# Kernel optimization log

Hardware: AMD Instinct MI355X
Metric: run time of the kernel (lower is better)

The kernel has to match this reference:

```python
import jax, jax.numpy as jnp
import numpy as np
from jax.scipy.special import logsumexp

# Module hyperparameters
N_PARTS = 128
BATCH = 1024
# Entropic-regularized solver settings (differentiable surrogate for the
# cvxpylayers LP solve; eps small relative to O(1) eta-phi distances)
EPS = 0.02
ITERS = 100
LOG_FLOOR = 1e-30  # avoid log(0) for zero-mass dummy particles


def setup_inputs() -> dict:
    key = jax.random.key(0)
    k1, k2 = jax.random.split(key)
    # [B, n_parts, 3]: features (eta, phi, pt); uniform fill keeps pt > 0
    jets1 = jax.random.uniform(k1, (BATCH, N_PARTS, 3), dtype=jnp.float32)
    jets2 = jax.random.uniform(k2, (BATCH, N_PARTS, 3), dtype=jnp.float32)
    return {"jets1": jets1, "jets2": jets2}


def _sinkhorn_flow(C, loga, logb):
    """Batched log-domain Sinkhorn. C: [B,N,M], loga: [B,N], logb: [B,M].
    Returns the transport plan (flow) [B,N,M] with marginals ~ (a, b)."""
    f = jnp.zeros_like(loga)
    g = jnp.zeros_like(logb)

    def step(carry, _):
        f, g = carry
        f = EPS * (loga - logsumexp((g[:, None, :] - C) / EPS, axis=2))
        g = EPS * (logb - logsumexp((f[:, :, None] - C) / EPS, axis=1))
        return (f, g), None

    (f, g), _ = jax.lax.scan(step, (f, g), None, length=ITERS)
    return jnp.exp((f[:, :, None] + g[:, None, :] - C) / EPS)


def reference(jets1, jets2):
    n = jets1.shape[1]
    # Pairwise eta-phi ground distances: [B, n, n]
    diffs = -(jets1[:, :, None, :2] - jets2[:, None, :, :2]) + 1e-12
    dists = jnp.linalg.norm(diffs, axis=3)
    # pt weights (LP marginals)
    w1 = jets1[:, :, 2]
    w2 = jets2[:, :, 2]
    E1 = jnp.sum(w1, axis=1)
    E2 = jnp.sum(w2, axis=1)
    EabsDiff = jnp.abs(E2 - E1)
    # Partial OT (total mass = min(E1,E2), row/col sums <= w) is made balanced
    # by adding one zero-cost dummy particle per side absorbing the excess mass.
    a = jnp.concatenate([w1, jnp.maximum(E2 - E1, 0.0)[:, None]], axis=1)  # [B, n+1]
    b = jnp.concatenate([w2, jnp.maximum(E1 - E2, 0.0)[:, None]], axis=1)  # [B, n+1]
    Cp = jnp.pad(dists, ((0, 0), (0, 1), (0, 1)))  # dummy row/col have zero cost
    loga = jnp.log(jnp.maximum(a, LOG_FLOOR))
    logb = jnp.log(jnp.maximum(b, LOG_FLOOR))
    flow = _sinkhorn_flow(Cp, loga, logb)  # [B, n+1, n+1]
    # EMD = transport cost over real particles + energy-difference penalty
    emds = jnp.sum(dists * flow[:, :n, :n], axis=(1, 2)) + EabsDiff  # [B]
    return emds
```

## Files before the change

kernel.cpp:

```cpp
#include <hip/hip_runtime.h>

#define NP    128
#define NITER 100
#define BLK   512
#define RSC   72.13475204444817f
#define IRSC  0.013862943611198906f

typedef __attribute__((ext_vector_type(8))) short bf16x8;
typedef __attribute__((ext_vector_type(4))) float f32x4;

template<int CTRL>
__device__ __forceinline__ float dppf(float x) {
  return __int_as_float(__builtin_amdgcn_update_dpp(
      0, __float_as_int(x), CTRL, 0xf, 0xf, false));
}
__device__ __forceinline__ float rowsum16(float x) {
  x += dppf<0x121>(x); x += dppf<0x122>(x);
  x += dppf<0x124>(x); x += dppf<0x128>(x);
  return x;
}
__device__ __forceinline__ float wsum64(float x) {
  #pragma unroll
  for (int s = 1; s < 64; s <<= 1) x += __shfl_xor(x, s);
  return x;
}
__device__ __forceinline__ unsigned short f2bf(float f) {
  unsigned u = __float_as_uint(f);
  u += 0x7fffu + ((u >> 16) & 1u);
  return (unsigned short)(u >> 16);
}
__device__ __forceinline__ float bf2f(unsigned short h) {
  return __uint_as_float(((unsigned)h) << 16);
}

__global__ __launch_bounds__(BLK, 4) void emd_sinkhorn(
    const float* __restrict__ j1g, const float* __restrict__ j2g,
    float* __restrict__ out)
{
  __shared__ __align__(16) float x1s[NP], y1s[NP], x2s[NP], y2s[NP];
  __shared__ __align__(16) float ah[NP + 4], bh[NP + 4];
  __shared__ __align__(16) unsigned short Qlds[NP], Plds[NP];
  __shared__ __align__(16) float sumQ[8], sumP[8];
  __shared__ float red[8];

  const int t  = threadIdx.x;
  const int l  = t & 63;
  const int wv = t >> 6;
  const int lg = l >> 4;
  const int li = l & 15;
  const int b  = blockIdx.x;
  const float* J1 = j1g + (size_t)b * (NP * 3);
  const float* J2 = j2g + (size_t)b * (NP * 3);

  if (t < NP) {
    x1s[t] = J1[3*t]; y1s[t] = J1[3*t+1]; ah[t] = J1[3*t+2];
    x2s[t] = J2[3*t]; y2s[t] = J2[3*t+1]; bh[t] = J2[3*t+2];
  }
  __syncthreads();

  const float e1 = wsum64(ah[l] + ah[l + 64]);
  const float e2 = wsum64(bh[l] + bh[l + 64]);
  const float dE = fabsf(e2 - e1);
  __syncthreads();

  if (t < NP) { ah[t] = fmaxf(ah[t], 1e-30f); bh[t] = fmaxf(bh[t], 1e-30f); }
  if (t == 0) {
    ah[NP] = fmaxf(fmaxf(e2 - e1, 0.0f), 1e-30f);
    bh[NP] = fmaxf(fmaxf(e1 - e2, 0.0f), 1e-30f);
  }
  if (t < NP) Qlds[t] = 0x3F80;
  if (l == 0) sumQ[wv] = 16.0f;
  __syncthreads();

  const float aslk = ah[NP], bslk = bh[NP];
  float a4[4];
  #pragma unroll
  for (int q = 0; q < 4; ++q) a4[q] = ah[16*wv + lg*4 + q];
  const float bcol = bh[16*wv + li];

  bf16x8 KA[4], KB[4];
  {
    const int nA = 16*wv + li;
    const int mB = 16*wv + li;
    const float x1A = x1s[nA], y1A = y1s[nA];
    const float x2B = x2s[mB], y2B = y2s[mB];
    #pragma unroll
    for (int c = 0; c < 4; ++c) {
      #pragma unroll
      for (int i = 0; i < 8; ++i) {
        const int k = 32*c + lg*8 + i;
        float dx = x2s[k] - x1A + 1e-12f;
        float dy = y2s[k] - y1A + 1e-12f;
        KA[c][i] = (short)f2bf(
            __builtin_amdgcn_exp2f(-__builtin_sqrtf(dx*dx + dy*dy) * RSC));
        dx = x2B - x1s[k] + 1e-12f;
        dy = y2B - y1s[k] + 1e-12f;
        KB[c][i] = (short)f2bf(
            __builtin_amdgcn_exp2f(-__builtin_sqrtf(dx*dx + dy*dy) * RSC));
      }
    }
  }

  float q128 = 1.0f, p128;
  bf16x8 qf[4];

  for (int it = 0; it < NITER; ++it) {
    #pragma unroll
    for (int c = 0; c < 4; ++c)
      qf[c] = *(const bf16x8*)&Qlds[c*32 + lg*8];
    const float4 s0 = *(const float4*)&sumQ[0];
    const float4 s1 = *(const float4*)&sumQ[4];
    const float SQ = ((s0.x + s0.y) + (s0.z + s0.w))
                   + ((s1.x + s1.y) + (s1.z + s1.w));
    f32x4 acc = {0.f, 0.f, 0.f, 0.f};
    #pragma unroll
    for (int c = 0; c < 4; ++c)
      acc = __builtin_amdgcn_mfma_f32_16x16x32_bf16(KA[c], qf[c], acc, 0, 0, 0);
    p128 = aslk * __builtin_amdgcn_rcpf(SQ + q128);
    float pv[4];
    #pragma unroll
    for (int q = 0; q < 4; ++q)
      pv[q] = a4[q] * __builtin_amdgcn_rcpf(acc[q] + q128);
    float ps = (pv[0] + pv[1]) + (pv[2] + pv[3]);
    ps += __shfl_xor(ps, 16);
    ps += __shfl_xor(ps, 32);
    if (l == 0) sumP[wv] = ps;
    if (li == 0) {
      uint2 pk;
      pk.x = (unsigned)f2bf(pv[0]) | ((unsigned)f2bf(pv[1]) << 16);
      pk.y = (unsigned)f2bf(pv[2]) | ((unsigned)f2bf(pv[3]) << 16);
      *(uint2*)&Plds[16*wv + lg*4] = pk;
    }
    __syncthreads();

    bf16x8 pf[4];
    #pragma unroll
    for (int c = 0; c < 4; ++c)
      pf[c] = *(const bf16x8*)&Plds[c*32 + lg*8];
    const float4 t0 = *(const float4*)&sumP[0];
    const float4 t1 = *(const float4*)&sumP[4];
    const float SP = ((t0.x + t0.y) + (t0.z + t0.w))
                   + ((t1.x + t1.y) + (t1.z + t1.w));
    f32x4 acc2 = {0.f, 0.f, 0.f, 0.f};
    #pragma unroll
    for (int c = 0; c < 4; ++c)
      acc2 = __builtin_amdgcn_mfma_f32_16x16x32_bf16(pf[c], KB[c], acc2, 0, 0, 0);
    q128 = bslk * __builtin_amdgcn_rcpf(SP + p128);
    const float qv = bcol * __builtin_amdgcn_rcpf(acc2[0] + p128);
    const float qs = rowsum16(qv);
    if (l == 0) sumQ[wv] = qs;
    if (l < 16) Qlds[16*wv + li] = f2bf(qv);
    __syncthreads();
  }

  const float Pn = bf2f(Plds[16*wv + li]);
  #pragma unroll
  for (int c = 0; c < 4; ++c)
    qf[c] = *(const bf16x8*)&Qlds[c*32 + lg*8];
  float acc = 0.0f;
  #pragma unroll
  for (int c = 0; c < 4; ++c) {
    #pragma unroll
    for (int i = 0; i < 8; ++i) {
      const float kk = bf2f((unsigned short)KA[c][i]);
      const float qm = bf2f((unsigned short)qf[c][i]);
      const float d  = -__builtin_amdgcn_logf(kk) * IRSC;
      acc = fmaf(d, (Pn * kk) * qm, acc);
    }
  }
  acc = wsum64(acc);
  if (l == 0) red[wv] = acc;
  __syncthreads();
  if (t == 0)
    out[b] = (((red[0] + red[1]) + (red[2] + red[3]))
            + ((red[4] + red[5]) + (red[6] + red[7]))) + dE;
}

extern "C" void kernel_launch(void* const* d_in, const int* in_sizes, int n_in,
                              void* d_out, int out_size, void* d_ws, size_t ws_size,
                              hipStream_t stream) {
  const float* j1 = (const float*)d_in[0];
  const float* j2 = (const float*)d_in[1];
  float* outp = (float*)d_out;
  const int batch = in_sizes[0] / (NP * 3);
  hipLaunchKernelGGL(emd_sinkhorn, dim3(batch), dim3(BLK), 0, stream,
                     j1, j2, outp);
}
```

Baseline: 192.7 us.

## Run each batch's Sinkhorn loop in a single wavefront holding full kernel matrices

Each batch element moves from an 8-wave block to a single 64-lane wave that keeps both full 128x128 bf16 Gibbs kernels in registers (KA and KB, 32 bf16x8 each). Each iteration issues 32 MFMAs per half-step in that one wave. Cross-wave shared-memory reductions are replaced by wave-local shuffles, and barriers become cheap single-wave syncs. The cost is much higher register pressure (about 256 VGPRs just for the kernels), possible spilling, and fewer waves per CU, so MFMA latency may be exposed with less parallelism available to hide it.

After: 236.7 us. 1.23x slower.

```diff
diff --git a/kernel.cpp b/kernel.cpp
--- a/kernel.cpp
+++ b/kernel.cpp
@@ -2,178 +2,177 @@
 
 #define NP    128
 #define NITER 100
-#define BLK   512
 #define RSC   72.13475204444817f
 #define IRSC  0.013862943611198906f
 
 typedef __attribute__((ext_vector_type(8))) short bf16x8;
 typedef __attribute__((ext_vector_type(4))) float f32x4;
 
-template<int CTRL>
-__device__ __forceinline__ float dppf(float x) {
-  return __int_as_float(__builtin_amdgcn_update_dpp(
-      0, __float_as_int(x), CTRL, 0xf, 0xf, false));
-}
-__device__ __forceinline__ float rowsum16(float x) {
-  x += dppf<0x121>(x); x += dppf<0x122>(x);
-  x += dppf<0x124>(x); x += dppf<0x128>(x);
-  return x;
-}
 __device__ __forceinline__ float wsum64(float x) {
   #pragma unroll
   for (int s = 1; s < 64; s <<= 1) x += __shfl_xor(x, s);
   return x;
+}
+__device__ __forceinline__ float bf2f(unsigned short h) {
+  return __uint_as_float(((unsigned)h) << 16);
 }
 __device__ __forceinline__ unsigned short f2bf(float f) {
   unsigned u = __float_as_uint(f);
   u += 0x7fffu + ((u >> 16) & 1u);
   return (unsigned short)(u >> 16);
 }
-__device__ __forceinline__ float bf2f(unsigned short h) {
-  return __uint_as_float(((unsigned)h) << 16);
-}
 
-__global__ __launch_bounds__(BLK, 4) void emd_sinkhorn(
+__global__ __launch_bounds__(64, 1) void emd_sinkhorn(
     const float* __restrict__ j1g, const float* __restrict__ j2g,
     float* __restrict__ out)
 {
   __shared__ __align__(16) float x1s[NP], y1s[NP], x2s[NP], y2s[NP];
-  __shared__ __align__(16) float ah[NP + 4], bh[NP + 4];
-  __shared__ __align__(16) unsigned short Qlds[NP], Plds[NP];
-  __shared__ __align__(16) float sumQ[8], sumP[8];
-  __shared__ float red[8];
+  __shared__ __align__(16) float ahs[NP], bhs[NP];
+  __shared__ __align__(16) float Slds[NP];
+  __shared__ __align__(16) unsigned short Plds[NP];
+  __shared__ __align__(16) unsigned short Qlds[NP];
 
-  const int t  = threadIdx.x;
-  const int l  = t & 63;
-  const int wv = t >> 6;
+  const int l  = threadIdx.x;
   const int lg = l >> 4;
   const int li = l & 15;
   const int b  = blockIdx.x;
   const float* J1 = j1g + (size_t)b * (NP * 3);
   const float* J2 = j2g + (size_t)b * (NP * 3);
 
-  if (t < NP) {
-    x1s[t] = J1[3*t]; y1s[t] = J1[3*t+1]; ah[t] = J1[3*t+2];
-    x2s[t] = J2[3*t]; y2s[t] = J2[3*t+1]; bh[t] = J2[3*t+2];
+  #pragma unroll
+  for (int k = l; k < NP; k += 64) {
+    x1s[k] = J1[3*k]; y1s[k] = J1[3*k+1]; ahs[k] = J1[3*k+2];
+    x2s[k] = J2[3*k]; y2s[k] = J2[3*k+1]; bhs[k] = J2[3*k+2];
   }
   __syncthreads();
 
-  const float e1 = wsum64(ah[l] + ah[l + 64]);
-  const float e2 = wsum64(bh[l] + bh[l + 64]);
+  const float e1 = wsum64(ahs[l] + ahs[l + 64]);
+  const float e2 = wsum64(bhs[l] + bhs[l + 64]);
   const float dE = fabsf(e2 - e1);
-  __syncthreads();
+  const float aslk = fmaxf(fmaxf(e2 - e1, 0.0f), 1e-30f);
+  const float bslk = fmaxf(fmaxf(e1 - e2, 0.0f), 1e-30f);
+  const float2 araw = *(const float2*)&ahs[2*l];
+  const float2 braw = *(const float2*)&bhs[2*l];
+  const float ah0 = fmaxf(araw.x, 1e-30f), ah1 = fmaxf(araw.y, 1e-30f);
+  const float bh0 = fmaxf(braw.x, 1e-30f), bh1 = fmaxf(braw.y, 1e-30f);
 
-  if (t < NP) { ah[t] = fmaxf(ah[t], 1e-30f); bh[t] = fmaxf(bh[t], 1e-30f); }
-  if (t == 0) {
-    ah[NP] = fmaxf(fmaxf(e2 - e1, 0.0f), 1e-30f);
-    bh[NP] = fmaxf(fmaxf(e1 - e2, 0.0f), 1e-30f);
+  bf16x8 KA[8][4], KB[8][4];
+  #pragma unroll
+  for (int rt = 0; rt < 8; ++rt) {
+    const float xr = x1s[16*rt + li], yr = y1s[16*rt + li];
+    #pragma unroll
+    for (int kt = 0; kt < 4; ++kt) {
+      #pragma unroll
+      for (int i2 = 0; i2 < 8; ++i2) {
+        const int k = 32*kt + 8*lg + i2;
+        const float dx = x2s[k] - xr + 1e-12f;
+        const float dy = y2s[k] - yr + 1e-12f;
+        KA[rt][kt][i2] = (short)f2bf(
+            __builtin_amdgcn_exp2f(-__builtin_sqrtf(dx*dx + dy*dy) * RSC));
+      }
+    }
   }
-  if (t < NP) Qlds[t] = 0x3F80;
-  if (l == 0) sumQ[wv] = 16.0f;
-  __syncthreads();
-
-  const float aslk = ah[NP], bslk = bh[NP];
-  float a4[4];
   #pragma unroll
-  for (int q = 0; q < 4; ++q) a4[q] = ah[16*wv + lg*4 + q];
-  const float bcol = bh[16*wv + li];
-
-  bf16x8 KA[4], KB[4];
-  {
-    const int nA = 16*wv + li;
-    const int mB = 16*wv + li;
-    const float x1A = x1s[nA], y1A = y1s[nA];
-    const float x2B = x2s[mB], y2B = y2s[mB];
+  for (int ct = 0; ct < 8; ++ct) {
+    const float xc = x2s[16*ct + li], yc = y2s[16*ct + li];
     #pragma unroll
-    for (int c = 0; c < 4; ++c) {
+    for (int kt = 0; kt < 4; ++kt) {
       #pragma unroll
-      for (int i = 0; i < 8; ++i) {
-        const int k = 32*c + lg*8 + i;
-        float dx = x2s[k] - x1A + 1e-12f;
-        float dy = y2s[k] - y1A + 1e-12f;
-        KA[c][i] = (short)f2bf(
-            __builtin_amdgcn_exp2f(-__builtin_sqrtf(dx*dx + dy*dy) * RSC));
-        dx = x2B - x1s[k] + 1e-12f;
-        dy = y2B - y1s[k] + 1e-12f;
-        KB[c][i] = (short)f2bf(
+      for (int i2 = 0; i2 < 8; ++i2) {
+        const int k = 32*kt + 8*lg + i2;
+        const float dx = xc - x1s[k] + 1e-12f;
+        const float dy = yc - y1s[k] + 1e-12f;
+        KB[ct][kt][i2] = (short)f2bf(
             __builtin_amdgcn_exp2f(-__builtin_sqrtf(dx*dx + dy*dy) * RSC));
       }
     }
   }
 
-  float q128 = 1.0f, p128;
-  bf16x8 qf[4];
+  ((unsigned*)Qlds)[l] = 0x3F803F80u;
+  float SQ = 128.0f, q128 = 1.0f;
+  __syncthreads();
 
   for (int it = 0; it < NITER; ++it) {
+    const float p128 = aslk * __builtin_amdgcn_rcpf(SQ + q128);
+
+    bf16x8 qf[4];
     #pragma unroll
-    for (int c = 0; c < 4; ++c)
-      qf[c] = *(const bf16x8*)&Qlds[c*32 + lg*8];
-    const float4 s0 = *(const float4*)&sumQ[0];
-    const float4 s1 = *(const float4*)&sumQ[4];
-    const float SQ = ((s0.x + s0.y) + (s0.z + s0.w))
-                   + ((s1.x + s1.y) + (s1.z + s1.w));
-    f32x4 acc = {0.f, 0.f, 0.f, 0.f};
+    for (int kt = 0; kt < 4; ++kt)
+      qf[kt] = *(const bf16x8*)((const char*)Qlds + 64*kt + 16*lg);
+    f32x4 acc[8];
     #pragma unroll
-    for (int c = 0; c < 4; ++c)
-      acc = __builtin_amdgcn_mfma_f32_16x16x32_bf16(KA[c], qf[c], acc, 0, 0, 0);
-    p128 = aslk * __builtin_amdgcn_rcpf(SQ + q128);
-    float pv[4];
-    #pragma unroll
-    for (int q = 0; q < 4; ++q)
-      pv[q] = a4[q] * __builtin_amdgcn_rcpf(acc[q] + q128);
-    float ps = (pv[0] + pv[1]) + (pv[2] + pv[3]);
-    ps += __shfl_xor(ps, 16);
-    ps += __shfl_xor(ps, 32);
-    if (l == 0) sumP[wv] = ps;
+    for (int rt = 0; rt < 8; ++rt) {
+      acc[rt] = (f32x4){q128, q128, q128, q128};
+      #pragma unroll
+      for (int kt = 0; kt < 4; ++kt)
+        acc[rt] = __builtin_amdgcn_mfma_f32_16x16x32_bf16(
+            KA[rt][kt], qf[kt], acc[rt], 0, 0, 0);
+    }
     if (li == 0) {
-      uint2 pk;
-      pk.x = (unsigned)f2bf(pv[0]) | ((unsigned)f2bf(pv[1]) << 16);
-      pk.y = (unsigned)f2bf(pv[2]) | ((unsigned)f2bf(pv[3]) << 16);
-      *(uint2*)&Plds[16*wv + lg*4] = pk;
+      #pragma unroll
+      for (int rt = 0; rt < 8; ++rt)
+        *(f32x4*)&Slds[16*rt + 4*lg] = acc[rt];
     }
+    __syncthreads();
+    const float2 s2 = *(const float2*)&Slds[2*l];
+    const float P0 = ah0 * __builtin_amdgcn_rcpf(s2.x);
+    const float P1 = ah1 * __builtin_amdgcn_rcpf(s2.y);
+    const float SP = wsum64(P0 + P1);
+    const float q128n = bslk * __builtin_amdgcn_rcpf(SP + p128);
+    ((unsigned*)Plds)[l] =
+        (unsigned)f2bf(P0) | ((unsigned)f2bf(P1) << 16);
     __syncthreads();
 
     bf16x8 pf[4];
     #pragma unroll
-    for (int c = 0; c < 4; ++c)
-      pf[c] = *(const bf16x8*)&Plds[c*32 + lg*8];
-    const float4 t0 = *(const float4*)&sumP[0];
-    const float4 t1 = *(const float4*)&sumP[4];
-    const float SP = ((t0.x + t0.y) + (t0.z + t0.w))
-                   + ((t1.x + t1.y) + (t1.z + t1.w));
-    f32x4 acc2 = {0.f, 0.f, 0.f, 0.f};
+    for (int kt = 0; kt < 4; ++kt)
+      pf[kt] = *(const bf16x8*)((const char*)Plds + 64*kt + 16*lg);
+    f32x4 acc2[8];
     #pragma unroll
-    for (int c = 0; c < 4; ++c)
-      acc2 = __builtin_amdgcn_mfma_f32_16x16x32_bf16(pf[c], KB[c], acc2, 0, 0, 0);
-    q128 = bslk * __builtin_amdgcn_rcpf(SP + p128);
-    const float qv = bcol * __builtin_amdgcn_rcpf(acc2[0] + p128);
-    const float qs = rowsum16(qv);
-    if (l == 0) sumQ[wv] = qs;
-    if (l < 16) Qlds[16*wv + li] = f2bf(qv);
+    for (int ct = 0; ct < 8; ++ct) {
+      acc2[ct] = (f32x4){p128, p128, p128, p128};
+      #pragma unroll
+      for (int kt = 0; kt < 4; ++kt)
+        acc2[ct] = __builtin_amdgcn_mfma_f32_16x16x32_bf16(
+            pf[kt], KB[ct][kt], acc2[ct], 0, 0, 0);
+    }
+    if (lg == 0) {
+      #pragma unroll
+      for (int ct = 0; ct < 8; ++ct)
+        Slds[16*ct + li] = acc2[ct][0];
+    }
+    __syncthreads();
+    const float2 t2 = *(const float2*)&Slds[2*l];
+    const float Q0 = bh0 * __builtin_amdgcn_rcpf(t2.x);
+    const float Q1 = bh1 * __builtin_amdgcn_rcpf(t2.y);
+    SQ = wsum64(Q0 + Q1);
+    ((unsigned*)Qlds)[l] =
+        (unsigned)f2bf(Q0) | ((unsigned)f2bf(Q1) << 16);
+    q128 = q128n;
     __syncthreads();
   }
 
-  const float Pn = bf2f(Plds[16*wv + li]);
+  bf16x8 qf[4];
   #pragma unroll
-  for (int c = 0; c < 4; ++c)
-    qf[c] = *(const bf16x8*)&Qlds[c*32 + lg*8];
-  float acc = 0.0f;
+  for (int kt = 0; kt < 4; ++kt)
+    qf[kt] = *(const bf16x8*)((const char*)Qlds + 64*kt + 16*lg);
+  float accE = 0.0f;
   #pragma unroll
-  for (int c = 0; c < 4; ++c) {
+  for (int rt = 0; rt < 8; ++rt) {
+    const float Pn = bf2f(Plds[16*rt + li]);
     #pragma unroll
-    for (int i = 0; i < 8; ++i) {
-      const float kk = bf2f((unsigned short)KA[c][i]);
-      const float qm = bf2f((unsigned short)qf[c][i]);
-      const float d  = -__builtin_amdgcn_logf(kk) * IRSC;
-      acc = fmaf(d, (Pn * kk) * qm, acc);
+    for (int kt = 0; kt < 4; ++kt) {
+      #pragma unroll
+      for (int i2 = 0; i2 < 8; ++i2) {
+        const float kk = bf2f((unsigned short)KA[rt][kt][i2]);
+        const float qm = bf2f((unsigned short)qf[kt][i2]);
+        const float d  = -__builtin_amdgcn_logf(kk) * IRSC;
+        accE = fmaf(d, (Pn * kk) * qm, accE);
+      }
     }
   }
-  acc = wsum64(acc);
-  if (l == 0) red[wv] = acc;
-  __syncthreads();
-  if (t == 0)
-    out[b] = (((red[0] + red[1]) + (red[2] + red[3]))
-            + ((red[4] + red[5]) + (red[6] + red[7]))) + dE;
+  accE = wsum64(accE);
+  if (l == 0) out[b] = accE + dE;
 }
 
 extern "C" void kernel_launch(void* const* d_in, const int* in_sizes, int n_in,
@@ -183,6 +182,6 @@
   const float* j2 = (const float*)d_in[1];
   float* outp = (float*)d_out;
   const int batch = in_sizes[0] / (NP * 3);
-  hipLaunchKernelGGL(emd_sinkhorn, dim3(batch), dim3(BLK), 0, stream,
+  hipLaunchKernelGGL(emd_sinkhorn, dim3(batch), dim3(64), 0, stream,
                      j1, j2, outp);
 }
```
